# Kernel tuning notes

Hardware: AMD Instinct MI355X
Metric: run time of the kernel (lower is better)

The kernel has to match this reference:

```python
import jax, jax.numpy as jnp
import numpy as np

HIDDEN = 2048
NUM_HEADS = 16
HEAD_DIM = HIDDEN // NUM_HEADS  # 128
LATENT = HIDDEN // 8            # 256
ROPE_THETA = 100000.0


def setup_inputs() -> dict:
    key = jax.random.key(0)
    ks = jax.random.split(key, 7)
    s = 0.02
    x = jax.random.normal(ks[0], (4, 1024, HIDDEN), dtype=jnp.float32)
    # weights stored as [in, out] (transpose of torch nn.Linear.weight)
    w_q_down = jax.random.normal(ks[1], (HIDDEN, LATENT), dtype=jnp.float32) * s
    w_kv_down = jax.random.normal(ks[2], (HIDDEN, LATENT), dtype=jnp.float32) * s
    w_q_up = jax.random.normal(ks[3], (LATENT, HIDDEN), dtype=jnp.float32) * s
    w_k_up = jax.random.normal(ks[4], (LATENT, HIDDEN), dtype=jnp.float32) * s
    w_v_up = jax.random.normal(ks[5], (LATENT, HIDDEN), dtype=jnp.float32) * s
    w_o = jax.random.normal(ks[6], (HIDDEN, HIDDEN), dtype=jnp.float32) * s
    return {"x": x, "w_q_down": w_q_down, "w_kv_down": w_kv_down,
            "w_q_up": w_q_up, "w_k_up": w_k_up, "w_v_up": w_v_up, "w_o": w_o}


def _rope_cos_sin(seq_len, dtype):
    # Llama rotary: inv_freq over even dims, emb = concat(freqs, freqs)
    inv_freq = 1.0 / (ROPE_THETA ** (jnp.arange(0, HEAD_DIM, 2, dtype=jnp.float32) / HEAD_DIM))
    pos = jnp.arange(seq_len, dtype=jnp.float32)
    freqs = pos[:, None] * inv_freq[None, :]          # [S, D/2]
    emb = jnp.concatenate([freqs, freqs], axis=-1)    # [S, D]
    return jnp.cos(emb).astype(dtype), jnp.sin(emb).astype(dtype)


def _rotate_half(t):
    h = t.shape[-1] // 2
    return jnp.concatenate([-t[..., h:], t[..., :h]], axis=-1)


def reference(x, w_q_down, w_kv_down, w_q_up, w_k_up, w_v_up, w_o):
    B, S, H = x.shape
    q_latent = x @ w_q_down                 # [B,S,latent]
    kv_latent = x @ w_kv_down               # [B,S,latent]
    q = (q_latent @ w_q_up).reshape(B, S, NUM_HEADS, HEAD_DIM)
    k = (kv_latent @ w_k_up).reshape(B, S, NUM_HEADS, HEAD_DIM)
    v = (kv_latent @ w_v_up).reshape(B, S, NUM_HEADS, HEAD_DIM)

    cos, sin = _rope_cos_sin(S, x.dtype)    # [S,D]
    cos = cos[None, :, None, :]             # [1,S,1,D] (unsqueeze_dim=2)
    sin = sin[None, :, None, :]
    q = q * cos + _rotate_half(q) * sin
    k = k * cos + _rotate_half(k) * sin

    # [B,H,S,D]
    q = q.transpose(0, 2, 1, 3)
    k = k.transpose(0, 2, 1, 3)
    v = v.transpose(0, 2, 1, 3)

    scale = 1.0 / jnp.sqrt(jnp.asarray(HEAD_DIM, dtype=x.dtype))
    scores = jnp.einsum('bhqd,bhkd->bhqk', q, k) * scale
    causal = jnp.tril(jnp.ones((S, S), dtype=bool))
    scores = jnp.where(causal[None, None], scores, jnp.finfo(scores.dtype).min)
    probs = jax.nn.softmax(scores, axis=-1)
    attn = jnp.einsum('bhqk,bhkd->bhqd', probs, v)  # [B,H,S,D]
    attn = attn.transpose(0, 2, 1, 3).reshape(B, S, H)
    return attn @ w_o
```

## Files before the change

kernel.cpp:

```cpp
#include <hip/hip_runtime.h>
#include <hip/hip_bf16.h>

typedef unsigned short u16;
typedef unsigned int u32;
typedef __attribute__((ext_vector_type(8))) __bf16 bf16x8;
typedef __attribute__((ext_vector_type(4))) float f32x4;

#define HID 2048
#define NH 16
#define HD 128
#define LAT 256
#define BATCH 4
#define SEQ 1024

__device__ __forceinline__ u16 f2bf(float f) {
  union { float f; u32 u; } v; v.f = f;
  u32 r = v.u + 0x7fffu + ((v.u >> 16) & 1u);
  return (u16)(r >> 16);
}

typedef const __attribute__((address_space(1))) u32 as1_u32;
typedef __attribute__((address_space(3))) u32 as3_u32;

__device__ __forceinline__ void load_lds16(const void* g, void* l) {
  __builtin_amdgcn_global_load_lds((as1_u32*)g, (as3_u32*)l, 16, 0, 0);
}

template<int WM, int WN, int MR, int NR>
__device__ __forceinline__ void gemm_core(const u16* __restrict__ A, const u16* __restrict__ Bt,
    int K, int lda, int ldb, int arow0, int brow0, u16* As, u16* Bs, f32x4 acc[MR][NR]) {
  constexpr int BM = WM * MR * 16, BN = WN * NR * 16;
  constexpr int NW = WM * WN;
  constexpr int ACH = (BM * 32) / 512;
  constexpr int BCH = (BN * 32) / 512;
  const int tid = threadIdx.x;
  const int lane = tid & 63, wave = tid >> 6;
  const int wm = wave % WM, wn = wave / WM;
  const int fr = lane & 15, fq = lane >> 4;

  for (int kt = 0; kt < K; kt += 32) {
    __syncthreads();
    #pragma unroll
    for (int cc = 0; cc < ACH / NW; ++cc) {
      int c = wave + cc * NW;
      int r = c * 16 + (lane >> 2);
      int col = (lane & 3) * 8;
      load_lds16(&A[(size_t)(arow0 + r) * lda + kt + col], &As[c * 512]);
    }
    #pragma unroll
    for (int cc = 0; cc < BCH / NW; ++cc) {
      int c = wave + cc * NW;
      int r = c * 16 + (lane >> 2);
      int col = (lane & 3) * 8;
      load_lds16(&Bt[(size_t)(brow0 + r) * ldb + kt + col], &Bs[c * 512]);
    }
    asm volatile("s_waitcnt vmcnt(0)" ::: "memory");
    __syncthreads();
    bf16x8 af[MR], bfr[NR];
    #pragma unroll
    for (int m = 0; m < MR; ++m)
      af[m] = *(const bf16x8*)&As[(wm * MR * 16 + m * 16 + fr) * 32 + fq * 8];
    #pragma unroll
    for (int n = 0; n < NR; ++n)
      bfr[n] = *(const bf16x8*)&Bs[(wn * NR * 16 + n * 16 + fr) * 32 + fq * 8];
    #pragma unroll
    for (int m = 0; m < MR; ++m)
      #pragma unroll
      for (int n = 0; n < NR; ++n)
        acc[m][n] = __builtin_amdgcn_mfma_f32_16x16x32_bf16(af[m], bfr[n], acc[m][n], 0, 0, 0);
  }
}

__global__ void __launch_bounds__(256) k_cvt(const float* __restrict__ in, u16* __restrict__ o, int n4) {
  int i = blockIdx.x * blockDim.x + threadIdx.x;
  if (i < n4) {
    float4 v = ((const float4*)in)[i];
    union { u16 s[4]; uint2 u; } w;
    w.s[0] = f2bf(v.x); w.s[1] = f2bf(v.y); w.s[2] = f2bf(v.z); w.s[3] = f2bf(v.w);
    ((uint2*)o)[i] = w.u;
  }
}

__global__ void __launch_bounds__(256) k_transpose3(const float* __restrict__ in0,
    const float* __restrict__ in1, const float* __restrict__ in2,
    u16* __restrict__ o0, u16* __restrict__ o1, u16* __restrict__ o2, int R, int C) {
  __shared__ float t[32][33];
  const float* in = blockIdx.z == 0 ? in0 : (blockIdx.z == 1 ? in1 : in2);
  u16* o = blockIdx.z == 0 ? o0 : (blockIdx.z == 1 ? o1 : o2);
  int bx = blockIdx.x * 32, by = blockIdx.y * 32;
  int tx = threadIdx.x, ty = threadIdx.y;
  #pragma unroll
  for (int i = ty; i < 32; i += 8) t[i][tx] = in[(size_t)(by + i) * C + bx + tx];
  __syncthreads();
  #pragma unroll
  for (int i = ty; i < 32; i += 8) o[(size_t)(bx + i) * R + by + tx] = f2bf(t[tx][i]);
}

__global__ void __launch_bounds__(256) k_cossin(float* __restrict__ cosT, float* __restrict__ sinT) {
  int idx = blockIdx.x * 256 + threadIdx.x;
  int s = idx >> 6, d = idx & 63;
  float inv = powf(100000.0f, -(float)d / 64.0f);
  float a = (float)s * inv;
  cosT[idx] = cosf(a);
  sinT[idx] = sinf(a);
}

__global__ void __launch_bounds__(256) k_down(const u16* __restrict__ xb, const u16* __restrict__ wqdT,
    const u16* __restrict__ wkvdT, u16* __restrict__ ql, u16* __restrict__ kvl) {
  __shared__ __align__(16) u16 As[128 * 32];
  __shared__ __align__(16) u16 Bs[64 * 32];
  const u16* Bt = blockIdx.z ? wkvdT : wqdT;
  u16* out = blockIdx.z ? kvl : ql;
  const int rb = blockIdx.x * 128, cb = blockIdx.y * 64;
  f32x4 acc[2][4] = {};
  gemm_core<4, 1, 2, 4>(xb, Bt, HID, HID, HID, rb, cb, As, Bs, acc);
  const int lane = threadIdx.x & 63, wave = threadIdx.x >> 6;
  const int fr = lane & 15, fq = lane >> 4;
  #pragma unroll
  for (int m = 0; m < 2; ++m)
    #pragma unroll
    for (int n = 0; n < 4; ++n)
      #pragma unroll
      for (int i = 0; i < 4; ++i)
        out[(size_t)(rb + wave * 32 + m * 16 + fq * 4 + i) * LAT + cb + n * 16 + fr] =
            f2bf(acc[m][n][i]);
}

__global__ void __launch_bounds__(256) k_up(const u16* __restrict__ ql, const u16* __restrict__ kvl,
    const u16* __restrict__ wquT, const u16* __restrict__ wkuT, const u16* __restrict__ wvuT,
    u16* __restrict__ q, u16* __restrict__ k, u16* __restrict__ vt,
    const float* __restrict__ cosT, const float* __restrict__ sinT) {
  __shared__ __align__(16) u16 As[128 * 32];
  __shared__ __align__(16) u16 Bs[128 * 32];
  const int mode = blockIdx.z;
  const u16* A = (mode == 0) ? ql : kvl;
  const u16* Bt = (mode == 0) ? wquT : (mode == 1 ? wkuT : wvuT);
  const int rb = blockIdx.x * 128;
  const int h = blockIdx.y;
  f32x4 acc[2][8] = {};
  gemm_core<4, 1, 2, 8>(A, Bt, LAT, LAT, LAT, rb, h * HD, As, Bs, acc);
  const int lane = threadIdx.x & 63, wave = threadIdx.x >> 6;
  const int fr = lane & 15, fq = lane >> 4;
  if (mode == 2) {
    #pragma unroll
    for (int m = 0; m < 2; ++m)
      #pragma unroll
      for (int n = 0; n < 8; ++n)
        #pragma unroll
        for (int i = 0; i < 4; ++i) {
          int row = rb + wave * 32 + m * 16 + fq * 4 + i;
          int b = row >> 10, s = row & 1023;
          int sp = (s & ~63) | (((s & 15) << 2) | ((s >> 4) & 3));
          vt[(size_t)((b * NH + h) * HD + n * 16 + fr) * SEQ + sp] = f2bf(acc[m][n][i]);
        }
  } else {
    u16* dst = (mode == 0) ? q : k;
    const float scale = (mode == 0) ? 0.08838834764831845f * 1.4426950408889634f : 1.0f;
    #pragma unroll
    for (int m = 0; m < 2; ++m)
      #pragma unroll
      for (int i = 0; i < 4; ++i) {
        int row = rb + wave * 32 + m * 16 + fq * 4 + i;
        int b = row >> 10, s = row & 1023;
        size_t base = (size_t)((b * NH + h) * SEQ + s) * HD;
        #pragma unroll
        for (int j = 0; j < 4; ++j) {
          int dlo = j * 16 + fr;
          float c = cosT[s * 64 + dlo], sn = sinT[s * 64 + dlo];
          float x1 = acc[m][j][i], x2 = acc[m][j + 4][i];
          dst[base + dlo] = f2bf((x1 * c - x2 * sn) * scale);
          dst[base + dlo + 64] = f2bf((x2 * c + x1 * sn) * scale);
        }
      }
  }
}

__global__ void __launch_bounds__(512, 2) k_attn(const u16* __restrict__ Q, const u16* __restrict__ Kc,
    const u16* __restrict__ Vt, u16* __restrict__ O) {
  __shared__ __align__(16) u16 Ks[2][64 * 128];
  __shared__ __align__(16) u16 Vs[2][128 * 64];
  __shared__ __align__(16) u16 Ps[8][16 * 64];
  const int f = blockIdx.x;
  const int bh = (f & 7) * 8 + (f >> 5);
  const int j = (f >> 3) & 3;
  const int h = bh & (NH - 1), b = bh >> 4;
  const int tid = threadIdx.x, lane = tid & 63, wave = tid >> 6;
  const int fr = lane & 15, fq = lane >> 4;
  const size_t qkb = (size_t)bh * SEQ * HD;
  const char* Kbase = (const char*)Kc + qkb * 2;
  const char* Vbase = (const char*)Vt + (size_t)bh * HD * SEQ * 2;

  const int qx0 = j, qx1 = 7 - j;
  const int nkt0 = 2 * qx0 + 2;
  const int total = 18;

  auto stage = [&](int buf, int t) {
    int kt = (t < nkt0) ? t : (t - nkt0);
    #pragma unroll
    for (int cc = 0; cc < 2; ++cc) {
      int c = wave * 2 + cc;
      int L = c * 1024 + lane * 16;
      int Lk = L ^ (((L >> 8) & 7) << 4);
      load_lds16(Kbase + (size_t)kt * 16384 + Lk, (char*)Ks[buf] + c * 1024);
      int Lv = L ^ (((L >> 7) & 7) << 4);
      int rv = Lv >> 7, colb = Lv & 127;
      load_lds16(Vbase + (size_t)rv * (SEQ * 2) + (size_t)kt * 128 + colb, (char*)Vs[buf] + c * 1024);
    }
  };

  bf16x8 ones;
  #pragma unroll
  for (int z = 0; z < 8; ++z) ones[z] = (__bf16)1.0f;

  bf16x8 qf[4];
  f32x4 ao[8];
  f32x4 lacc;
  int qw = qx0 * 128 + wave * 16;

  auto loadQ = [&]() {
    #pragma unroll
    for (int c = 0; c < 4; ++c)
      qf[c] = *(const bf16x8*)&Q[qkb + (size_t)(qw + fr) * HD + c * 32 + fq * 8];
  };
  auto reset = [&]() {
    f32x4 z = {};
    #pragma unroll
    for (int jj = 0; jj < 8; ++jj) ao[jj] = z;
    lacc = z;
  };
  auto epi = [&]() {
    #pragma unroll
    for (int i = 0; i < 4; ++i) {
      float inv = 1.f / lacc[i];
      int s = qw + fq * 4 + i;
      size_t base = (size_t)(b * SEQ + s) * HID + h * HD;
      #pragma unroll
      for (int jj = 0; jj < 8; ++jj)
        O[base + jj * 16 + fr] = f2bf(ao[jj][i] * inv);
    }
  };

  loadQ();
  reset();
  stage(0, 0);
  asm volatile("s_waitcnt vmcnt(0)" ::: "memory");
  __syncthreads();

  int cur = 0;
  for (int t = 0; t < total; ++t) {
    if (t + 1 < total) stage(cur ^ 1, t + 1);
    if (t == nkt0) {
      epi();
      qw = qx1 * 128 + wave * 16;
      loadQ();
      reset();
    }
    const int ktp = (t < nkt0) ? t : (t - nkt0);
    const int k0 = ktp * 64;
    if (k0 <= qw + 15) {
      f32x4 sc[4] = {};
      #pragma unroll
      for (int c = 0; c < 4; ++c)
        #pragma unroll
        for (int n = 0; n < 4; ++n) {
          int rr = n * 16 + fr;
          int off = (rr * 256 + c * 64 + fq * 16) ^ ((rr & 7) << 4);
          bf16x8 kf = *(const bf16x8*)((const char*)Ks[cur] + off);
          sc[n] = __builtin_amdgcn_mfma_f32_16x16x32_bf16(qf[c], kf, sc[n], 0, 0, 0);
        }

      const bool needmask = (k0 + 63 > qw);
      #pragma unroll
      for (int i = 0; i < 4; ++i) {
        int row = qw + fq * 4 + i;
        float p[4];
        #pragma unroll
        for (int n = 0; n < 4; ++n) {
          float sv = sc[n][i];
          if (needmask) sv = (k0 + n * 16 + fr <= row) ? sv : -1e30f;
          p[n] = exp2f(sv);
        }
        u32 w0, w1;
        asm("v_cvt_pk_bf16_f32 %0, %1, %2" : "=v"(w0) : "v"(p[0]), "v"(p[1]));
        asm("v_cvt_pk_bf16_f32 %0, %1, %2" : "=v"(w1) : "v"(p[2]), "v"(p[3]));
        int prow = fq * 4 + i;
        int o = (prow * 128 + fr * 8) ^ ((prow & 7) << 4);
        *(uint2*)((char*)Ps[wave] + o) = make_uint2(w0, w1);
      }

      bf16x8 pa[2];
      #pragma unroll
      for (int kf = 0; kf < 2; ++kf) {
        int off = (fr * 128 + kf * 64 + fq * 16) ^ ((fr & 7) << 4);
        pa[kf] = *(const bf16x8*)((const char*)Ps[wave] + off);
      }
      lacc = __builtin_amdgcn_mfma_f32_16x16x32_bf16(pa[0], ones, lacc, 0, 0, 0);
      lacc = __builtin_amdgcn_mfma_f32_16x16x32_bf16(pa[1], ones, lacc, 0, 0, 0);
      #pragma unroll
      for (int jj = 0; jj < 8; ++jj)
        #pragma unroll
        for (int kf = 0; kf < 2; ++kf) {
          int rv = jj * 16 + fr;
          int off = (rv * 128 + kf * 64 + fq * 16) ^ ((rv & 7) << 4);
          bf16x8 vf = *(const bf16x8*)((const char*)Vs[cur] + off);
          ao[jj] = __builtin_amdgcn_mfma_f32_16x16x32_bf16(pa[kf], vf, ao[jj], 0, 0, 0);
        }
    }
    asm volatile("s_waitcnt vmcnt(0)" ::: "memory");
    __syncthreads();
    cur ^= 1;
  }
  epi();
}

__global__ void __launch_bounds__(256) k_out(const u16* __restrict__ at, const u16* __restrict__ woT,
    float* __restrict__ out) {
  __shared__ __align__(16) u16 As[128 * 128];
  __shared__ __align__(16) u16 Bs[128 * 128];
  const int rb = blockIdx.x * 128, cb = blockIdx.y * 128;
  const int tid = threadIdx.x, lane = tid & 63, wave = tid >> 6;
  const int wm = wave & 1, wn = wave >> 1;
  const int fr = lane & 15, fq = lane >> 4;
  const char* Ab = (const char*)at;
  const char* Bb = (const char*)woT;

  f32x4 acc[4][4] = {};

  for (int kt = 0; kt < HID; kt += 128) {
    __syncthreads();
    #pragma unroll
    for (int cc = 0; cc < 8; ++cc) {
      int c = wave * 8 + cc;
      int L = c * 1024 + lane * 16;
      int Ls = L ^ (((L >> 8) & 7) << 4);
      int r = Ls >> 8, colb = Ls & 255;
      load_lds16(Ab + (size_t)(rb + r) * (HID * 2) + kt * 2 + colb, (char*)As + c * 1024);
      load_lds16(Bb + (size_t)(cb + r) * (HID * 2) + kt * 2 + colb, (char*)Bs + c * 1024);
    }
    asm volatile("s_waitcnt vmcnt(0)" ::: "memory");
    __syncthreads();

    #pragma unroll
    for (int kk = 0; kk < 4; ++kk) {
      bf16x8 af[4], bfr[4];
      #pragma unroll
      for (int m = 0; m < 4; ++m) {
        int r = wm * 64 + m * 16 + fr;
        af[m] = *(const bf16x8*)((const char*)As + ((r * 256 + kk * 64 + fq * 16) ^ ((r & 7) << 4)));
      }
      #pragma unroll
      for (int n = 0; n < 4; ++n) {
        int r = wn * 64 + n * 16 + fr;
        bfr[n] = *(const bf16x8*)((const char*)Bs + ((r * 256 + kk * 64 + fq * 16) ^ ((r & 7) << 4)));
      }
      #pragma unroll
      for (int m = 0; m < 4; ++m)
        #pragma unroll
        for (int n = 0; n < 4; ++n)
          acc[m][n] = __builtin_amdgcn_mfma_f32_16x16x32_bf16(af[m], bfr[n], acc[m][n], 0, 0, 0);
    }
  }

  #pragma unroll
  for (int m = 0; m < 4; ++m)
    #pragma unroll
    for (int n = 0; n < 4; ++n)
      #pragma unroll
      for (int i = 0; i < 4; ++i)
        out[(size_t)(rb + wm * 64 + m * 16 + fq * 4 + i) * HID + cb + wn * 64 + n * 16 + fr] =
            acc[m][n][i];
}

extern "C" void kernel_launch(void* const* d_in, const int* in_sizes, int n_in,
                              void* d_out, int out_size, void* d_ws, size_t ws_size,
                              hipStream_t stream) {
  const float* x    = (const float*)d_in[0];
  const float* wqd  = (const float*)d_in[1];
  const float* wkvd = (const float*)d_in[2];
  const float* wqu  = (const float*)d_in[3];
  const float* wku  = (const float*)d_in[4];
  const float* wvu  = (const float*)d_in[5];
  const float* wo   = (const float*)d_in[6];
  float* out = (float*)d_out;

  char* p = (char*)d_ws;
  u16* xb    = (u16*)(p + 0);
  u16* at    = xb;
  u16* wqdT  = (u16*)(p + 16777216);
  u16* wkvdT = (u16*)(p + 17825792);
  u16* wquT  = (u16*)(p + 18874368);
  u16* wkuT  = (u16*)(p + 19922944);
  u16* wvuT  = (u16*)(p + 20971520);
  u16* woT   = (u16*)(p + 22020096);
  u16* ql    = (u16*)(p + 30408704);
  u16* kvl   = (u16*)(p + 32505856);
  u16* q     = (u16*)(p + 34603008);
  u16* kk    = (u16*)(p + 51380224);
  u16* vt    = (u16*)(p + 68157440);
  float* cosT = (float*)(p + 84934656);
  float* sinT = (float*)(p + 85196800);

  k_cvt<<<8192, 256, 0, stream>>>(x, xb, 2097152);
  k_transpose3<<<dim3(8, 64, 2), dim3(32, 8), 0, stream>>>(wqd, wkvd, wkvd, wqdT, wkvdT, wkvdT, 2048, 256);
  k_transpose3<<<dim3(64, 8, 3), dim3(32, 8), 0, stream>>>(wqu, wku, wvu, wquT, wkuT, wvuT, 256, 2048);
  k_transpose3<<<dim3(64, 64, 1), dim3(32, 8), 0, stream>>>(wo, wo, wo, woT, woT, woT, 2048, 2048);
  k_cossin<<<256, 256, 0, stream>>>(cosT, sinT);

  k_down<<<dim3(32, 4, 2), 256, 0, stream>>>(xb, wqdT, wkvdT, ql, kvl);
  k_up<<<dim3(32, 16, 3), 256, 0, stream>>>(ql, kvl, wquT, wkuT, wvuT, q, kk, vt, cosT, sinT);
  k_attn<<<256, 512, 0, stream>>>(q, kk, vt, at);
  k_out<<<dim3(32, 16), 256, 0, stream>>>(at, woT, out);
}
```

Before: 168.7 us.

## Double-buffer out-projection GEMM and relax attention load waits with partial vmcnt

The output-projection GEMM now splits K into 64-wide stages and double-buffers them in LDS, so the global-to-LDS load of the next stage overlaps with the MFMA work on the current one. The attention loop issues the next K/V stage first and then waits only for the older loads (partial vmcnt count) before a raw s_barrier, rather than fully draining loads at the end of each iteration. This targets exposed global-load latency in both kernels. The hard-coded vmcnt counts must match the exact number of loads each stage issues, so a miscount could allow reads of stale LDS data.

```diff
diff --git a/kernel.cpp b/kernel.cpp
--- a/kernel.cpp
+++ b/kernel.cpp
@@ -243,12 +243,17 @@
   loadQ();
   reset();
   stage(0, 0);
-  asm volatile("s_waitcnt vmcnt(0)" ::: "memory");
-  __syncthreads();
 
   int cur = 0;
   for (int t = 0; t < total; ++t) {
-    if (t + 1 < total) stage(cur ^ 1, t + 1);
+    if (t + 1 < total) {
+      stage(cur ^ 1, t + 1);
+      asm volatile("s_waitcnt vmcnt(4)" ::: "memory");
+    } else {
+      asm volatile("s_waitcnt vmcnt(0)" ::: "memory");
+    }
+    asm volatile("s_barrier" ::: "memory");
+
     if (t == nkt0) {
       epi();
       qw = qx1 * 128 + wave * 16;
@@ -306,8 +311,7 @@
           ao[jj] = __builtin_amdgcn_mfma_f32_16x16x32_bf16(pa[kf], vf, ao[jj], 0, 0, 0);
         }
     }
-    asm volatile("s_waitcnt vmcnt(0)" ::: "memory");
-    __syncthreads();
+    asm volatile("s_barrier" ::: "memory");
     cur ^= 1;
   }
   epi();
@@ -315,8 +319,8 @@
 
 __global__ void __launch_bounds__(256) k_out(const u16* __restrict__ at, const u16* __restrict__ woT,
     float* __restrict__ out) {
-  __shared__ __align__(16) u16 As[128 * 128];
-  __shared__ __align__(16) u16 Bs[128 * 128];
+  __shared__ __align__(16) u16 As[2][128 * 64];
+  __shared__ __align__(16) u16 Bs[2][128 * 64];
   const int rb = blockIdx.x * 128, cb = blockIdx.y * 128;
   const int tid = threadIdx.x, lane = tid & 63, wave = tid >> 6;
   const int wm = wave & 1, wn = wave >> 1;
@@ -326,32 +330,41 @@
 
   f32x4 acc[4][4] = {};
 
-  for (int kt = 0; kt < HID; kt += 128) {
-    __syncthreads();
-    #pragma unroll
-    for (int cc = 0; cc < 8; ++cc) {
-      int c = wave * 8 + cc;
+  auto stage = [&](int buf, int s) {
+    #pragma unroll
+    for (int cc = 0; cc < 4; ++cc) {
+      int c = wave * 4 + cc;
       int L = c * 1024 + lane * 16;
-      int Ls = L ^ (((L >> 8) & 7) << 4);
-      int r = Ls >> 8, colb = Ls & 255;
-      load_lds16(Ab + (size_t)(rb + r) * (HID * 2) + kt * 2 + colb, (char*)As + c * 1024);
-      load_lds16(Bb + (size_t)(cb + r) * (HID * 2) + kt * 2 + colb, (char*)Bs + c * 1024);
-    }
-    asm volatile("s_waitcnt vmcnt(0)" ::: "memory");
-    __syncthreads();
-
-    #pragma unroll
-    for (int kk = 0; kk < 4; ++kk) {
+      int Ls = L ^ (((L >> 7) & 7) << 4);
+      int r = Ls >> 7, colb = Ls & 127;
+      load_lds16(Ab + (size_t)(rb + r) * (HID * 2) + s * 128 + colb, (char*)As[buf] + c * 1024);
+      load_lds16(Bb + (size_t)(cb + r) * (HID * 2) + s * 128 + colb, (char*)Bs[buf] + c * 1024);
+    }
+  };
+
+  stage(0, 0);
+  int buf = 0;
+  for (int s = 0; s < 32; ++s) {
+    if (s + 1 < 32) {
+      stage(buf ^ 1, s + 1);
+      asm volatile("s_waitcnt vmcnt(8)" ::: "memory");
+    } else {
+      asm volatile("s_waitcnt vmcnt(0)" ::: "memory");
+    }
+    asm volatile("s_barrier" ::: "memory");
+
+    #pragma unroll
+    for (int kk = 0; kk < 2; ++kk) {
       bf16x8 af[4], bfr[4];
       #pragma unroll
       for (int m = 0; m < 4; ++m) {
         int r = wm * 64 + m * 16 + fr;
-        af[m] = *(const bf16x8*)((const char*)As + ((r * 256 + kk * 64 + fq * 16) ^ ((r & 7) << 4)));
+        af[m] = *(const bf16x8*)((const char*)As[buf] + ((r * 128 + kk * 64 + fq * 16) ^ ((r & 7) << 4)));
       }
       #pragma unroll
       for (int n = 0; n < 4; ++n) {
         int r = wn * 64 + n * 16 + fr;
-        bfr[n] = *(const bf16x8*)((const char*)Bs + ((r * 256 + kk * 64 + fq * 16) ^ ((r & 7) << 4)));
+        bfr[n] = *(const bf16x8*)((const char*)Bs[buf] + ((r * 128 + kk * 64 + fq * 16) ^ ((r & 7) << 4)));
       }
       #pragma unroll
       for (int m = 0; m < 4; ++m)
@@ -359,6 +372,9 @@
         for (int n = 0; n < 4; ++n)
           acc[m][n] = __builtin_amdgcn_mfma_f32_16x16x32_bf16(af[m], bfr[n], acc[m][n], 0, 0, 0);
     }
+
+    asm volatile("s_barrier" ::: "memory");
+    buf ^= 1;
   }
 
   #pragma unroll
```

Result: slower. 174.7 us (+3.5%).
